# Kernel optimization log

Measured on AMD Instinct MI355X. Metric: run time of the kernel, lower is better.

The kernel has to match this reference:

```python
import jax, jax.numpy as jnp
import numpy as np

N = 20000   # nodes per type per hop
E = 200000  # edges per relation per hop
H = 512     # node_feature_hid_len
FU = 512    # raw user feature len
FI = 256    # raw item feature len
NUM_RES = 2
NUM_DNN = 2


def setup_inputs() -> dict:
    key = jax.random.key(0)
    ks = iter(jax.random.split(key, 64))
    p = lambda shape: jax.random.normal(next(ks), shape, dtype=jnp.float32) * 0.05
    inp = {}
    # features per hop per type
    for h in range(3):
        inp[f'feat_user_h{h}'] = jax.random.normal(next(ks), (N, FU), dtype=jnp.float32)
        inp[f'feat_item_h{h}'] = jax.random.normal(next(ks), (N, FI), dtype=jnp.float32)
    del inp['feat_user_h2_']; 


def _unused():
    pass

# rebuild setup_inputs cleanly (above stub replaced)

def setup_inputs() -> dict:
    key = jax.random.key(0)
    ks = iter(jax.random.split(key, 64))
    p = lambda shape: jax.random.normal(next(ks), shape, dtype=jnp.float32) * 0.05
    inp = {}
    for h in range(3):
        inp[f'feat_user_h{h}'] = jax.random.normal(next(ks), (N, FU), dtype=jnp.float32)
        inp[f'feat_item_h{h}'] = jax.random.normal(next(ks), (N, FI), dtype=jnp.float32)
    for name in ('edges_UI_h0', 'edges_IU_h0', 'edges_UI_h1', 'edges_IU_h1'):
        inp[name] = jax.random.randint(next(ks), (2, E), 0, N, dtype=jnp.int32)
    # per-node-type input transforms
    inp['W_user'] = p((FU, H)); inp['b_user'] = jnp.zeros((H,), jnp.float32)
    inp['W_item'] = p((FI, H)); inp['b_item'] = jnp.zeros((H,), jnp.float32)
    # per-relation GATConv params, stacked over 2 relations [UI, IU]
    inp['gat_feat_W'] = p((2, H, H)); inp['gat_feat_b'] = jnp.zeros((2, H), jnp.float32)
    inp['gat_att_w'] = p((2, 2 * H)); inp['gat_att_b'] = jnp.zeros((2,), jnp.float32)
    inp['gat_bias'] = jnp.zeros((2, H), jnp.float32)
    # Res_DNN params
    inp['prep_W'] = p((H, H)); inp['prep_b'] = jnp.zeros((H,), jnp.float32)
    inp['dnn_W'] = p((NUM_RES, NUM_DNN, H, H)); inp['dnn_b'] = jnp.zeros((NUM_RES, NUM_DNN, H), jnp.float32)
    inp['dnn_ln_g'] = jnp.ones((NUM_RES, NUM_DNN, H), jnp.float32); inp['dnn_ln_b'] = jnp.zeros((NUM_RES, NUM_DNN, H), jnp.float32)
    inp['res_ln_g'] = jnp.ones((NUM_RES, H), jnp.float32); inp['res_ln_b'] = jnp.zeros((NUM_RES, H), jnp.float32)
    inp['cls_W'] = p((H, 1)); inp['cls_b'] = jnp.zeros((1,), jnp.float32)
    return inp


def _ln(x, g, b, eps=1e-5):
    mu = jnp.mean(x, axis=-1, keepdims=True)
    var = jnp.mean((x - mu) ** 2, axis=-1, keepdims=True)
    return (x - mu) * jax.lax.rsqrt(var + eps) * g + b


def _gat(head_h, tail_h, edges, fW, fb, aw, ab, bias):
    # GATConv: feat_linear on both sides, tanh edge attention, per-source-row
    # sparse softmax, scatter-weighted sum of transformed tail features.
    s = head_h @ fW + fb            # [Nh, H]
    t = tail_h @ fW + fb            # [Nt, H]
    src, tgt = edges[0], edges[1]
    # att(cat([s_e, t_e])) split into per-node scores (same math as concat @ aw)
    e = jnp.tanh((s @ aw[:H])[src] + (t @ aw[H:])[tgt] + ab)  # [E]
    nh = head_h.shape[0]
    m = jax.ops.segment_max(e, src, num_segments=nh)
    ex = jnp.exp(e - m[src])
    den = jax.ops.segment_sum(ex, src, num_segments=nh)
    alpha = ex / den[src]
    hp = jax.ops.segment_sum(alpha[:, None] * t[tgt], src, num_segments=nh)
    return hp + bias


def _forward(feat_user_h0, feat_item_h0, feat_user_h1, feat_item_h1,
             feat_user_h2, feat_item_h2,
             W_user, b_user, W_item, b_item,
             gat_feat_W, gat_feat_b, gat_att_w, gat_att_b, gat_bias,
             prep_W, prep_b, dnn_W, dnn_b, dnn_ln_g, dnn_ln_b,
             res_ln_g, res_ln_b, cls_W, cls_b,
             edges_UI_h0, edges_IU_h0, edges_UI_h1, edges_IU_h1):
    def gat(r, head, tail, edges):
        return _gat(head, tail, edges, gat_feat_W[r], gat_feat_b[r],
                    gat_att_w[r], gat_att_b[r], gat_bias[r])
    # hop 2 (deepest): transformed source features
    su = feat_user_h2 @ W_user + b_user
    si = feat_item_h2 @ W_item + b_item
    # hop 1
    hu = feat_user_h1 @ W_user + b_user
    hi = feat_item_h1 @ W_item + b_item
    su_new = (hu + gat(0, hu, si, edges_UI_h1)) * 0.5  # mean of [self, UI agg]
    si_new = (hi + gat(1, hi, su, edges_IU_h1)) * 0.5
    su, si = su_new, si_new
    # hop 0
    hu = feat_user_h0 @ W_user + b_user
    hi = feat_item_h0 @ W_item + b_item
    su_new = (hu + gat(0, hu, si, edges_UI_h0)) * 0.5
    su = su_new  # target node type = 'user' (first key)
    # Res_DNN head
    x = su @ prep_W + prep_b
    for r in range(NUM_RES):
        sc = x
        for d in range(NUM_DNN):
            x = _ln(jnp.tanh(x @ dnn_W[r, d] + dnn_b[r, d]), dnn_ln_g[r, d], dnn_ln_b[r, d])
        x = _ln(jnp.tanh(sc + x), res_ln_g[r], res_ln_b[r])
    return jax.nn.sigmoid(x @ cls_W + cls_b)  # [N, 1]


def reference(feat_user_h0, feat_item_h0, feat_user_h1, feat_item_h1,
              feat_user_h2, feat_item_h2,
              edges_UI_h0, edges_IU_h0, edges_UI_h1, edges_IU_h1,
              W_user, b_user, W_item, b_item,
              gat_feat_W, gat_feat_b, gat_att_w, gat_att_b, gat_bias,
              prep_W, prep_b, dnn_W, dnn_b, dnn_ln_g, dnn_ln_b,
              res_ln_g, res_ln_b, cls_W, cls_b):
    return _forward(feat_user_h0, feat_item_h0, feat_user_h1, feat_item_h1,
                    feat_user_h2, feat_item_h2,
                    W_user, b_user, W_item, b_item,
                    gat_feat_W, gat_feat_b, gat_att_w, gat_att_b, gat_bias,
                    prep_W, prep_b, dnn_W, dnn_b, dnn_ln_g, dnn_ln_b,
                    res_ln_g, res_ln_b, cls_W, cls_b,
                    edges_UI_h0, edges_IU_h0, edges_UI_h1, edges_IU_h1)
```

## Files before the change

### kernel.cpp

```cpp
#include <hip/hip_runtime.h>
#include <math.h>

#define NN 20000
#define NE 200000
#define HH 512

typedef __attribute__((ext_vector_type(8))) short short8v;
typedef __attribute__((ext_vector_type(4))) float f32x4;

__device__ inline short f2bf(float f) {
    union { float f; unsigned u; } v; v.f = f;
    unsigned r = (v.u + 0x7fffu + ((v.u >> 16) & 1u)) >> 16;
    return (short)r;
}
__device__ inline float bf2f(short s) {
    union { unsigned u; float f; } v;
    v.u = ((unsigned)(unsigned short)s) << 16;
    return v.f;
}

__device__ inline void gload_lds16(const void* g, void* l) {
    __builtin_amdgcn_global_load_lds(
        (const __attribute__((address_space(1))) void*)g,
        (__attribute__((address_space(3))) void*)l, 16, 0, 0);
}

__global__ __launch_bounds__(256)
void f2b_kernel(const float* __restrict__ src, short* __restrict__ dst, int n8)
{
    int i = blockIdx.x * 256 + threadIdx.x;
    if (i >= n8) return;
    const float4* p = (const float4*)src + (size_t)i * 2;
    float4 a = p[0], b = p[1];
    short8v s;
    s[0] = f2bf(a.x); s[1] = f2bf(a.y); s[2] = f2bf(a.z); s[3] = f2bf(a.w);
    s[4] = f2bf(b.x); s[5] = f2bf(b.y); s[6] = f2bf(b.z); s[7] = f2bf(b.w);
    ((short8v*)dst)[i] = s;
}

__global__ __launch_bounds__(256)
void wtr_kernel(const float* __restrict__ src, short* __restrict__ dst,
                int K, int Ncols)
{
    __shared__ float t[32][33];
    int bx = blockIdx.x * 32;
    int by = blockIdx.y * 32;
    int tx = threadIdx.x, ty = threadIdx.y;
    for (int i = ty; i < 32; i += 8)
        t[i][tx] = src[(size_t)(by + i) * Ncols + bx + tx];
    __syncthreads();
    for (int i = ty; i < 32; i += 8)
        dst[(size_t)(bx + i) * K + by + tx] = f2bf(t[tx][i]);
}

__global__ __launch_bounds__(256)
void mfma_lin(const short* __restrict__ X, const short* __restrict__ WT,
              const float* __restrict__ bias, float* __restrict__ outF,
              short* __restrict__ outB, int M, int K)
{
    __shared__ short8v As[2][512];
    __shared__ short8v Bs[2][512];

    const int tid = threadIdx.x;
    const int lane = tid & 63;
    const int w = tid >> 6;

    const int nby = (M + 127) >> 7;
    const int nwg = nby << 2;
    const int q = nwg >> 3, r = nwg & 7;
    int id = blockIdx.x;
    int xcd = id & 7, wi = id >> 3;
    int wgid = (xcd < r ? xcd * (q + 1) : r * (q + 1) + (xcd - r) * q) + wi;
    const int col0 = (wgid & 3) * 128;
    const int row0 = (wgid >> 2) * 128;

    const int wr = (w >> 1) * 64;
    const int wc = (w & 1) * 64;

    int sp0 = w * 128 + lane;
    int sp1 = sp0 + 64;
    int r0_ = sp0 >> 2, r1_ = sp1 >> 2;
    int c0_ = (sp0 & 3) ^ ((r0_ >> 1) & 3);
    int c1_ = (sp1 & 3) ^ ((r1_ >> 1) & 3);
    int ga0 = row0 + r0_; if (ga0 >= M) ga0 = M - 1;
    int ga1 = row0 + r1_; if (ga1 >= M) ga1 = M - 1;
    const short* ag0 = X + (size_t)ga0 * K + c0_ * 8;
    const short* ag1 = X + (size_t)ga1 * K + c1_ * 8;
    const short* bg0 = WT + (size_t)(col0 + r0_) * K + c0_ * 8;
    const short* bg1 = WT + (size_t)(col0 + r1_) * K + c1_ * 8;

    int ar[4], br[4];
#pragma unroll
    for (int i = 0; i < 4; ++i) {
        int rr = wr + i * 16 + (lane & 15);
        ar[i] = rr * 4 + ((lane >> 4) ^ ((rr >> 1) & 3));
        int nn = wc + i * 16 + (lane & 15);
        br[i] = nn * 4 + ((lane >> 4) ^ ((nn >> 1) & 3));
    }

    f32x4 acc[4][4];
#pragma unroll
    for (int i = 0; i < 4; ++i)
#pragma unroll
        for (int j = 0; j < 4; ++j)
            acc[i][j] = (f32x4){0.f, 0.f, 0.f, 0.f};

    auto stage = [&](int buf, int kk) {
        gload_lds16(ag0 + kk, &As[buf][sp0 & ~63]);
        gload_lds16(ag1 + kk, &As[buf][sp1 & ~63]);
        gload_lds16(bg0 + kk, &Bs[buf][sp0 & ~63]);
        gload_lds16(bg1 + kk, &Bs[buf][sp1 & ~63]);
    };

    const int nt = K >> 5;
    stage(0, 0);
    __syncthreads();
    int cur = 0;
    for (int t = 0; t < nt; ++t) {
        if (t + 1 < nt) stage(cur ^ 1, (t + 1) * 32);
        short8v af[4], bf[4];
#pragma unroll
        for (int i = 0; i < 4; ++i) af[i] = As[cur][ar[i]];
#pragma unroll
        for (int j = 0; j < 4; ++j) bf[j] = Bs[cur][br[j]];
#pragma unroll
        for (int i = 0; i < 4; ++i)
#pragma unroll
            for (int j = 0; j < 4; ++j)
                acc[i][j] = __builtin_amdgcn_mfma_f32_16x16x32_bf16(af[i], bf[j], acc[i][j], 0, 0, 0);
        __syncthreads();
        cur ^= 1;
    }

    float bj[4];
#pragma unroll
    for (int j = 0; j < 4; ++j)
        bj[j] = bias[col0 + wc + j * 16 + (lane & 15)];
#pragma unroll
    for (int i = 0; i < 4; ++i) {
#pragma unroll
        for (int rr = 0; rr < 4; ++rr) {
            int row = row0 + wr + i * 16 + (lane >> 4) * 4 + rr;
            if (row < M) {
                size_t base = (size_t)row * HH + col0 + wc + (lane & 15);
                if (outF) {
                    float* op = outF + base;
#pragma unroll
                    for (int j = 0; j < 4; ++j) op[j * 16] = acc[i][j][rr] + bj[j];
                }
                if (outB) {
                    short* op = outB + base;
#pragma unroll
                    for (int j = 0; j < 4; ++j) op[j * 16] = f2bf(acc[i][j][rr] + bj[j]);
                }
            }
        }
    }
}

__global__ __launch_bounds__(256)
void gat_pre_kernel(const float* __restrict__ fW, const float* __restrict__ fb,
                    const float* __restrict__ aw, float* __restrict__ uv,
                    float* __restrict__ s0t0)
{
    int row = blockIdx.x * 4 + (threadIdx.x >> 6);
    int lane = threadIdx.x & 63;
    const float4* ah = (const float4*)aw;
    const float4* at = (const float4*)(aw + HH);
    const float4* fp;
    if (row < 512)      fp = (const float4*)(fW + (size_t)row * HH);
    else if (row == 512) fp = (const float4*)fb;
    else return;
    float du = 0.f, dv = 0.f;
#pragma unroll
    for (int l = 0; l < 2; ++l) {
        int idx = lane * 2 + l;
        float4 f = fp[idx], a = ah[idx], b = at[idx];
        du += f.x*a.x + f.y*a.y + f.z*a.z + f.w*a.w;
        dv += f.x*b.x + f.y*b.y + f.z*b.z + f.w*b.w;
    }
#pragma unroll
    for (int m = 32; m >= 1; m >>= 1) {
        du += __shfl_xor(du, m);
        dv += __shfl_xor(dv, m);
    }
    if (lane == 0) {
        if (row < 512) { uv[row] = du; uv[512 + row] = dv; }
        else           { s0t0[0] = du; s0t0[1] = dv; }
    }
}

__global__ __launch_bounds__(256)
void rowdot2_kernel(const short* __restrict__ Hd, const short* __restrict__ Tl,
                    const float* __restrict__ uv, const float* __restrict__ s0t0,
                    float* __restrict__ ss, float* __restrict__ ts, int N)
{
    int row = blockIdx.x * 4 + (threadIdx.x >> 6);
    int lane = threadIdx.x & 63;
    if (row >= N) return;
    short8v h = ((const short8v*)(Hd + (size_t)row * HH))[lane];
    short8v t = ((const short8v*)(Tl + (size_t)row * HH))[lane];
    const float4* up = (const float4*)uv + lane * 2;
    const float4* vp = (const float4*)(uv + HH) + lane * 2;
    float4 u0 = up[0], u1 = up[1], v0 = vp[0], v1 = vp[1];
    float a = bf2f(h[0])*u0.x + bf2f(h[1])*u0.y + bf2f(h[2])*u0.z + bf2f(h[3])*u0.w
            + bf2f(h[4])*u1.x + bf2f(h[5])*u1.y + bf2f(h[6])*u1.z + bf2f(h[7])*u1.w;
    float b = bf2f(t[0])*v0.x + bf2f(t[1])*v0.y + bf2f(t[2])*v0.z + bf2f(t[3])*v0.w
            + bf2f(t[4])*v1.x + bf2f(t[5])*v1.y + bf2f(t[6])*v1.z + bf2f(t[7])*v1.w;
#pragma unroll
    for (int m = 32; m >= 1; m >>= 1) {
        a += __shfl_xor(a, m);
        b += __shfl_xor(b, m);
    }
    if (lane == 0) { ss[row] = a + s0t0[0]; ts[row] = b + s0t0[1]; }
}

__global__ __launch_bounds__(256)
void count2_kernel(const int* __restrict__ s0, const int* __restrict__ s1,
                   int* __restrict__ c0, int* __restrict__ c1, int E)
{
    int i = blockIdx.x * blockDim.x + threadIdx.x;
    if (i < E) atomicAdd(&c0[s0[i]], 1);
    else if (i < 2 * E) atomicAdd(&c1[s1[i - E]], 1);
}

__global__ __launch_bounds__(1024)
void scan2_kernel(const int* __restrict__ c0, const int* __restrict__ c1,
                  int* __restrict__ o0, int* __restrict__ o1,
                  int* __restrict__ u0, int* __restrict__ u1, int n)
{
    const int* counts = blockIdx.x ? c1 : c0;
    int* offs = blockIdx.x ? o1 : o0;
    int* curs = blockIdx.x ? u1 : u0;
    __shared__ int part[1024];
    const int tid = threadIdx.x;
    const int CH = (n + 1023) / 1024;
    const int base = tid * CH;
    int s = 0;
    for (int i = 0; i < CH; ++i) {
        int idx = base + i;
        if (idx < n) s += counts[idx];
    }
    part[tid] = s;
    __syncthreads();
    for (int d = 1; d < 1024; d <<= 1) {
        int v = 0;
        if (tid >= d) v = part[tid - d];
        __syncthreads();
        if (tid >= d) part[tid] += v;
        __syncthreads();
    }
    int run = (tid == 0) ? 0 : part[tid - 1];
    for (int i = 0; i < CH; ++i) {
        int idx = base + i;
        if (idx < n) { offs[idx] = run; curs[idx] = run; run += counts[idx]; }
    }
    if (tid == 1023) offs[n] = run;
}

__global__ __launch_bounds__(256)
void fill_kernel(const int* __restrict__ src, const int* __restrict__ tgt,
                 const float* __restrict__ ss, const float* __restrict__ ts,
                 const float* __restrict__ ab_ptr, int* __restrict__ cursor,
                 int* __restrict__ tvals, float* __restrict__ wv, int E)
{
    int i = blockIdx.x * blockDim.x + threadIdx.x;
    if (i >= E) return;
    int s = src[i], t = tgt[i];
    int pos = atomicAdd(&cursor[s], 1);
    tvals[pos] = t;
    wv[pos] = expf(tanhf(ss[s] + ts[t] + ab_ptr[0]));
}

__global__ __launch_bounds__(256)
void gat_agg_kernel(const int* __restrict__ offs, const int* __restrict__ tvals,
                    const float* __restrict__ wv, const short* __restrict__ T,
                    const short* __restrict__ head, const float* __restrict__ gbias,
                    short* __restrict__ out, int N)
{
    int s = blockIdx.x * 4 + (threadIdx.x >> 6);
    int lane = threadIdx.x & 63;
    if (s >= N) return;
    const int beg = offs[s], end = offs[s + 1];
    float a[8];
#pragma unroll
    for (int q = 0; q < 8; ++q) a[q] = 0.f;
    float den = 0.f;

    int j = beg;
    for (; j + 4 <= end; j += 4) {
        int t0 = tvals[j], t1 = tvals[j + 1], t2 = tvals[j + 2], t3 = tvals[j + 3];
        float w0 = wv[j], w1 = wv[j + 1], w2 = wv[j + 2], w3 = wv[j + 3];
        short8v v0 = ((const short8v*)(T + (size_t)t0 * HH))[lane];
        short8v v1 = ((const short8v*)(T + (size_t)t1 * HH))[lane];
        short8v v2 = ((const short8v*)(T + (size_t)t2 * HH))[lane];
        short8v v3 = ((const short8v*)(T + (size_t)t3 * HH))[lane];
        den += w0 + w1 + w2 + w3;
#pragma unroll
        for (int q = 0; q < 8; ++q) {
            float acc = a[q];
            acc = fmaf(w0, bf2f(v0[q]), acc);
            acc = fmaf(w1, bf2f(v1[q]), acc);
            acc = fmaf(w2, bf2f(v2[q]), acc);
            acc = fmaf(w3, bf2f(v3[q]), acc);
            a[q] = acc;
        }
    }
    for (; j < end; ++j) {
        int t = tvals[j];
        float w = wv[j];
        short8v tv = ((const short8v*)(T + (size_t)t * HH))[lane];
        den += w;
#pragma unroll
        for (int q = 0; q < 8; ++q) a[q] = fmaf(w, bf2f(tv[q]), a[q]);
    }
    float inv = (den > 0.f) ? 1.f / den : 0.f;

    short8v h = ((const short8v*)(head + (size_t)s * HH))[lane];
    const float4* bp = (const float4*)gbias + lane * 2;
    float4 b0 = bp[0], b1 = bp[1];
    float bb[8] = {b0.x, b0.y, b0.z, b0.w, b1.x, b1.y, b1.z, b1.w};
    short8v o;
#pragma unroll
    for (int q = 0; q < 8; ++q)
        o[q] = f2bf((bf2f(h[q]) + a[q] * inv + bb[q]) * 0.5f);
    ((short8v*)(out + (size_t)s * HH))[lane] = o;
}

__global__ __launch_bounds__(256)
void tanh_ln_kernel(const short* __restrict__ Z, const float* __restrict__ res,
                    const float* __restrict__ g, const float* __restrict__ bta,
                    short* __restrict__ outB, float* __restrict__ outF,
                    const float* __restrict__ cWp, const float* __restrict__ cbp,
                    float* __restrict__ outCls, int N)
{
    int row = blockIdx.x * 4 + (threadIdx.x >> 6);
    int lane = threadIdx.x & 63;
    if (row >= N) return;
    short8v zv = ((const short8v*)(Z + (size_t)row * HH))[lane];
    float v[8];
    float sum = 0.f, sum2 = 0.f;
    float rr[8];
    if (res) {
        const float4* rp = (const float4*)(res + (size_t)row * HH) + lane * 2;
        float4 r0 = rp[0], r1 = rp[1];
        rr[0]=r0.x; rr[1]=r0.y; rr[2]=r0.z; rr[3]=r0.w;
        rr[4]=r1.x; rr[5]=r1.y; rr[6]=r1.z; rr[7]=r1.w;
    } else {
#pragma unroll
        for (int q = 0; q < 8; ++q) rr[q] = 0.f;
    }
#pragma unroll
    for (int q = 0; q < 8; ++q) {
        float t = tanhf(bf2f(zv[q]) + rr[q]);
        v[q] = t;
        sum += t;
        sum2 = fmaf(t, t, sum2);
    }
#pragma unroll
    for (int m = 32; m >= 1; m >>= 1) {
        sum  += __shfl_xor(sum, m);
        sum2 += __shfl_xor(sum2, m);
    }
    float mu  = sum * (1.f/HH);
    float var = sum2 * (1.f/HH) - mu*mu;
    float rs  = rsqrtf(var + 1e-5f);
    const float4* gp = (const float4*)g + lane * 2;
    const float4* bp = (const float4*)bta + lane * 2;
    float4 g0 = gp[0], g1 = gp[1], c0 = bp[0], c1 = bp[1];
    float gg[8] = {g0.x, g0.y, g0.z, g0.w, g1.x, g1.y, g1.z, g1.w};
    float cc[8] = {c0.x, c0.y, c0.z, c0.w, c1.x, c1.y, c1.z, c1.w};
    float o[8];
#pragma unroll
    for (int q = 0; q < 8; ++q) o[q] = (v[q]-mu)*rs*gg[q] + cc[q];
    if (outB) {
        short8v ob;
#pragma unroll
        for (int q = 0; q < 8; ++q) ob[q] = f2bf(o[q]);
        ((short8v*)(outB + (size_t)row * HH))[lane] = ob;
    }
    if (outF) {
        float4* op = (float4*)(outF + (size_t)row * HH) + lane * 2;
        op[0] = make_float4(o[0], o[1], o[2], o[3]);
        op[1] = make_float4(o[4], o[5], o[6], o[7]);
    }
    if (cWp) {
        const float4* wp = (const float4*)cWp + lane * 2;
        float4 w0 = wp[0], w1 = wp[1];
        float acc = o[0]*w0.x + o[1]*w0.y + o[2]*w0.z + o[3]*w0.w
                  + o[4]*w1.x + o[5]*w1.y + o[6]*w1.z + o[7]*w1.w;
#pragma unroll
        for (int m = 32; m >= 1; m >>= 1) acc += __shfl_xor(acc, m);
        if (lane == 0) outCls[row] = 1.f / (1.f + expf(-(acc + cbp[0])));
    }
}

extern "C" void kernel_launch(void* const* d_in, const int* in_sizes, int n_in,
                              void* d_out, int out_size, void* d_ws, size_t ws_size,
                              hipStream_t stream)
{
    (void)in_sizes; (void)n_in; (void)out_size; (void)ws_size;
    const int N = NN, E = NE, H = HH;
    const size_t NHf = (size_t)N * H;

    const float* fu0 = (const float*)d_in[0];
    const float* fi1 = (const float*)d_in[3];
    const float* fu2 = (const float*)d_in[4];
    const int* eUI0 = (const int*)d_in[6];
    const int* eIU1 = (const int*)d_in[9];
    const float* Wu  = (const float*)d_in[10];
    const float* bu  = (const float*)d_in[11];
    const float* Wi  = (const float*)d_in[12];
    const float* bi  = (const float*)d_in[13];
    const float* gfW = (const float*)d_in[14];
    const float* gfb = (const float*)d_in[15];
    const float* gaw = (const float*)d_in[16];
    const float* gab = (const float*)d_in[17];
    const float* gbias = (const float*)d_in[18];
    const float* prW = (const float*)d_in[19];
    const float* prb = (const float*)d_in[20];
    const float* dW  = (const float*)d_in[21];
    const float* db  = (const float*)d_in[22];
    const float* dlg = (const float*)d_in[23];
    const float* dlb = (const float*)d_in[24];
    const float* rlg = (const float*)d_in[25];
    const float* rlb = (const float*)d_in[26];
    const float* cW  = (const float*)d_in[27];
    const float* cb  = (const float*)d_in[28];

    float* B5   = (float*)d_ws;
    float* ssb  = B5 + NHf;
    float* tsb  = ssb + N;
    float* uv   = tsb + N;
    float* s0t0 = uv + 1024;
    float* wvb  = s0t0 + 4;
    int* counts0 = (int*)(wvb + E);
    int* counts1 = counts0 + N;
    int* offs0   = counts1 + N;
    int* offs1   = offs0 + N + 1;
    int* cur0    = offs1 + N + 1;
    int* cur1    = cur0 + N;
    int* tvals   = cur1 + N;
    size_t boff = (size_t)((char*)(tvals + E) - (char*)d_ws);
    boff = (boff + 15) & ~(size_t)15;
    short* S0    = (short*)((char*)d_ws + boff);
    short* SUHU  = S0 + 2 * NHf;
    short* XI1   = SUHU + 2 * NHf;
    short* HI    = XI1 + NHf / 2;
    short* SINEW = HI + NHf;
    short* T4    = SINEW + NHf;
    short* SUF   = T4 + NHf;
    short* WTu   = SUF + NHf;
    short* WTi   = WTu + 512 * 512;
    short* WTg0  = WTi + 512 * 256;
    short* WTg1  = WTg0 + 512 * 512;
    short* WTpr  = WTg1 + 512 * 512;
    short* WTd   = WTpr + 512 * 512;
    short* SU  = SUHU;
    short* HU0 = SUHU + NHf;
    short* XB  = SINEW;
    short* ZB  = SU;

    auto WTR = [&](const float* src, short* dst, int K) {
        hipLaunchKernelGGL(wtr_kernel, dim3(16, K / 32), dim3(32, 8), 0, stream,
                           src, dst, K, 512);
    };
    WTR(Wu, WTu, 512);
    WTR(Wi, WTi, 256);
    WTR(gfW, WTg0, 512);
    WTR(gfW + (size_t)H * H, WTg1, 512);
    WTR(prW, WTpr, 512);
    for (int k = 0; k < 4; ++k)
        WTR(dW + (size_t)k * H * H, WTd + (size_t)k * 512 * 512, 512);

    auto F2B = [&](const float* src, short* dst, size_t n) {
        int n8 = (int)(n / 8);
        hipLaunchKernelGGL(f2b_kernel, dim3((n8 + 255) / 256), dim3(256), 0, stream,
                           src, dst, n8);
    };

    hipMemsetAsync(counts0, 0, 2 * N * sizeof(int), stream);
    hipLaunchKernelGGL(count2_kernel, dim3((2 * E + 255) / 256), dim3(256), 0, stream,
                       eUI0, eIU1, counts0, counts1, E);
    hipLaunchKernelGGL(scan2_kernel, dim3(2), dim3(1024), 0, stream,
                       counts0, counts1, offs0, offs1, cur0, cur1, N);

    auto MLIN = [&](const short* X, const short* WT, const float* b,
                    float* oF, short* oB, int M, int K) {
        int nwg = ((M + 127) / 128) * 4;
        hipLaunchKernelGGL(mfma_lin, dim3(nwg), dim3(256), 0, stream,
                           X, WT, b, oF, oB, M, K);
    };
    const int rgrid = (N + 3) / 4;
    const int egrid = (E + 255) / 256;

    auto GAT = [&](int r, const short* headB, const short* tailB, const short* WTg,
                   const int* edges, int* offs, int* curs, short* outB) {
        hipLaunchKernelGGL(gat_pre_kernel, dim3(130), dim3(256), 0, stream,
                           gfW + (size_t)r * H * H, gfb + r * H, gaw + (size_t)r * 2 * H,
                           uv, s0t0);
        MLIN(tailB, WTg, gfb + r * H, nullptr, T4, N, 512);
        hipLaunchKernelGGL(rowdot2_kernel, dim3(rgrid), dim3(256), 0, stream,
                           headB, tailB, uv, s0t0, ssb, tsb, N);
        hipLaunchKernelGGL(fill_kernel, dim3(egrid), dim3(256), 0, stream,
                           edges, edges + E, ssb, tsb, gab + r, curs, tvals, wvb, E);
        hipLaunchKernelGGL(gat_agg_kernel, dim3(rgrid), dim3(256), 0, stream,
                           offs, tvals, wvb, T4, headB, gbias + (size_t)r * H, outB, N);
    };

    F2B(fu2, S0, NHf);
    F2B(fu0, S0 + NHf, NHf);
    F2B(fi1, XI1, NHf / 2);
    MLIN(S0, WTu, bu, nullptr, SUHU, 2 * N, 512);
    MLIN(XI1, WTi, bi, nullptr, HI, N, 256);
    GAT(1, HI, SU, WTg1, eIU1, offs1, cur1, SINEW);
    GAT(0, HU0, SINEW, WTg0, eUI0, offs0, cur0, SUF);

    MLIN(SUF, WTpr, prb, B5, XB, N, 512);
    for (int r = 0; r < 2; ++r) {
        for (int d = 0; d < 2; ++d) {
            MLIN(XB, WTd + (size_t)(r * 2 + d) * 512 * 512, db + (r * 2 + d) * H,
                 nullptr, ZB, N, 512);
            hipLaunchKernelGGL(tanh_ln_kernel, dim3(rgrid), dim3(256), 0, stream,
                               ZB, (const float*)nullptr, dlg + (r * 2 + d) * H,
                               dlb + (r * 2 + d) * H, XB, (float*)nullptr,
                               (const float*)nullptr, (const float*)nullptr,
                               (float*)nullptr, N);
        }
        if (r == 0) {
            hipLaunchKernelGGL(tanh_ln_kernel, dim3(rgrid), dim3(256), 0, stream,
                               XB, B5, rlg, rlb, XB, B5,
                               (const float*)nullptr, (const float*)nullptr,
                               (float*)nullptr, N);
        } else {
            hipLaunchKernelGGL(tanh_ln_kernel, dim3(rgrid), dim3(256), 0, stream,
                               XB, B5, rlg + H, rlb + H, (short*)nullptr,
                               (float*)nullptr, cW, cb, (float*)d_out, N);
        }
    }
}
```

Before: 586.6 us.

## Triple-buffer GEMM LDS staging and vectorize bf16 epilogue via LDS

Moves the MFMA linear kernel from double to triple buffering over a shared LDS pool. Loads are issued two stages ahead, with explicit vmcnt waits and raw barriers replacing __syncthreads, so global-to-LDS latency overlaps more with compute. The bf16 output path now goes through a padded per-wave LDS tile and is written back as 16-byte vectors instead of scattered 2-byte stores. The cost is more LDS per block, which may lower occupancy, and the hand-set vmcnt counts must match the number of outstanding loads exactly.

Result: faster. 571.7 us (-2.5%).

```diff
diff --git a/kernel.cpp b/kernel.cpp
--- a/kernel.cpp
+++ b/kernel.cpp
@@ -58,8 +58,7 @@
               const float* __restrict__ bias, float* __restrict__ outF,
               short* __restrict__ outB, int M, int K)
 {
-    __shared__ short8v As[2][512];
-    __shared__ short8v Bs[2][512];
+    __shared__ short8v pool[3072];
 
     const int tid = threadIdx.x;
     const int lane = tid & 63;
@@ -106,53 +105,79 @@
             acc[i][j] = (f32x4){0.f, 0.f, 0.f, 0.f};
 
     auto stage = [&](int buf, int kk) {
-        gload_lds16(ag0 + kk, &As[buf][sp0 & ~63]);
-        gload_lds16(ag1 + kk, &As[buf][sp1 & ~63]);
-        gload_lds16(bg0 + kk, &Bs[buf][sp0 & ~63]);
-        gload_lds16(bg1 + kk, &Bs[buf][sp1 & ~63]);
+        short8v* A = pool + buf * 512;
+        short8v* B = pool + 1536 + buf * 512;
+        gload_lds16(ag0 + kk, A + w * 128);
+        gload_lds16(ag1 + kk, A + w * 128 + 64);
+        gload_lds16(bg0 + kk, B + w * 128);
+        gload_lds16(bg1 + kk, B + w * 128 + 64);
     };
 
     const int nt = K >> 5;
     stage(0, 0);
-    __syncthreads();
+    if (nt > 1) stage(1, 32);
+    if (nt > 2) stage(2, 64);
     int cur = 0;
     for (int t = 0; t < nt; ++t) {
-        if (t + 1 < nt) stage(cur ^ 1, (t + 1) * 32);
+        if (t + 2 < nt)      asm volatile("s_waitcnt vmcnt(8)" ::: "memory");
+        else if (t + 1 < nt) asm volatile("s_waitcnt vmcnt(4)" ::: "memory");
+        else                 asm volatile("s_waitcnt vmcnt(0)" ::: "memory");
+        __builtin_amdgcn_s_barrier();
+        const short8v* A = pool + cur * 512;
+        const short8v* B = pool + 1536 + cur * 512;
         short8v af[4], bf[4];
 #pragma unroll
-        for (int i = 0; i < 4; ++i) af[i] = As[cur][ar[i]];
-#pragma unroll
-        for (int j = 0; j < 4; ++j) bf[j] = Bs[cur][br[j]];
+        for (int i = 0; i < 4; ++i) af[i] = A[ar[i]];
+#pragma unroll
+        for (int j = 0; j < 4; ++j) bf[j] = B[br[j]];
 #pragma unroll
         for (int i = 0; i < 4; ++i)
 #pragma unroll
             for (int j = 0; j < 4; ++j)
                 acc[i][j] = __builtin_amdgcn_mfma_f32_16x16x32_bf16(af[i], bf[j], acc[i][j], 0, 0, 0);
-        __syncthreads();
-        cur ^= 1;
+        __builtin_amdgcn_s_barrier();
+        if (t + 3 < nt) stage(cur, (t + 3) * 32);
+        cur = (cur == 2) ? 0 : cur + 1;
     }
 
     float bj[4];
 #pragma unroll
     for (int j = 0; j < 4; ++j)
         bj[j] = bias[col0 + wc + j * 16 + (lane & 15)];
-#pragma unroll
-    for (int i = 0; i < 4; ++i) {
-#pragma unroll
-        for (int rr = 0; rr < 4; ++rr) {
-            int row = row0 + wr + i * 16 + (lane >> 4) * 4 + rr;
-            if (row < M) {
-                size_t base = (size_t)row * HH + col0 + wc + (lane & 15);
-                if (outF) {
-                    float* op = outF + base;
+
+    if (outF) {
+#pragma unroll
+        for (int i = 0; i < 4; ++i) {
+#pragma unroll
+            for (int rr = 0; rr < 4; ++rr) {
+                int row = row0 + wr + i * 16 + (lane >> 4) * 4 + rr;
+                if (row < M) {
+                    float* op = outF + (size_t)row * HH + col0 + wc + (lane & 15);
 #pragma unroll
                     for (int j = 0; j < 4; ++j) op[j * 16] = acc[i][j][rr] + bj[j];
                 }
-                if (outB) {
-                    short* op = outB + base;
-#pragma unroll
-                    for (int j = 0; j < 4; ++j) op[j * 16] = f2bf(acc[i][j][rr] + bj[j]);
-                }
+            }
+        }
+    }
+    if (outB) {
+        short* lds = (short*)pool + w * 4608;
+#pragma unroll
+        for (int i = 0; i < 4; ++i)
+#pragma unroll
+            for (int rr = 0; rr < 4; ++rr) {
+                int lrow = i * 16 + (lane >> 4) * 4 + rr;
+#pragma unroll
+                for (int j = 0; j < 4; ++j)
+                    lds[lrow * 72 + j * 16 + (lane & 15)] = f2bf(acc[i][j][rr] + bj[j]);
+            }
+#pragma unroll
+        for (int k = 0; k < 8; ++k) {
+            int lr = (lane >> 3) + 8 * k;
+            int lc = (lane & 7) * 8;
+            int grow = row0 + wr + lr;
+            if (grow < M) {
+                short8v vv = *(short8v*)(lds + lr * 72 + lc);
+                *(short8v*)(outB + (size_t)grow * HH + col0 + wc + lc) = vv;
             }
         }
     }
```
